# Kernel optimization log

Hardware: AMD Instinct MI355X
Metric: run time of the kernel (lower is better)

## Reference

```python
import jax, jax.numpy as jnp
import numpy as np

SIZES = [512, 2048, 4096, 8192, 16384]
BATCH = 64
MASK_DENSITY = 0.05  # GO DAG edge masks are very sparse


def setup_inputs() -> dict:
    key = jax.random.key(0)
    keys = jax.random.split(key, 1 + 3 * 4)
    inp = {"x": jax.random.normal(keys[0], (BATCH, SIZES[0]), dtype=jnp.float32)}
    for i in range(4):
        fan_in, fan_out = SIZES[i], SIZES[i + 1]
        scale = 1.0 / np.sqrt(fan_in)
        inp[f"W{i}"] = jax.random.normal(keys[1 + 3 * i], (fan_out, fan_in), dtype=jnp.float32) * scale
        inp[f"b{i}"] = jax.random.normal(keys[2 + 3 * i], (fan_out,), dtype=jnp.float32) * scale
        inp[f"mask{i}"] = jax.random.uniform(keys[3 + 3 * i], (fan_out, fan_in)) < MASK_DENSITY
    return inp


def reference(x, W0, W1, W2, W3, b0, b1, b2, b3, mask0, mask1, mask2, mask3):
    Ws = [W0, W1, W2, W3]
    bs = [b0, b1, b2, b3]
    masks = [mask0, mask1, mask2, mask3]
    n = len(Ws)
    for i in range(n):
        # SparseLinear: weight zeroed outside the GO parent-child edge mask
        Wm = Ws[i] * masks[i].astype(x.dtype)  # [out, in]
        x = x @ Wm.T + bs[i]                   # [B, out]
        if i < n - 1:
            x = jax.nn.relu(x)  # ReLU between all but the last layer
    return x
```

## Files before the change

kernel.cpp:

```cpp
#include <hip/hip_runtime.h>
#include <stdint.h>


typedef short bf16x8 __attribute__((ext_vector_type(8)));
typedef float f32x4  __attribute__((ext_vector_type(4)));

__device__ __forceinline__ unsigned short f2bf(float f) {
    unsigned int u = __float_as_uint(f);
    return (unsigned short)((u + 0x7FFFu + ((u >> 16) & 1u)) >> 16);
}

__device__ __forceinline__ unsigned int bfpair(float lo, float hi) {
    return (unsigned int)f2bf(lo) | ((unsigned int)f2bf(hi) << 16);
}

__device__ __forceinline__ bf16x8 pack8(const float4& a, const float4& b) {
    union { unsigned int u[4]; bf16x8 v; } r;
    r.u[0] = bfpair(a.x, a.y);
    r.u[1] = bfpair(a.z, a.w);
    r.u[2] = bfpair(b.x, b.y);
    r.u[3] = bfpair(b.z, b.w);
    return r.v;
}

__global__ __launch_bounds__(256) void probe_mask_kind(
    const unsigned int* __restrict__ m, int* __restrict__ flag)
{
    __shared__ int s_any;
    if (threadIdx.x == 0) s_any = 0;
    __syncthreads();
    int any = 0;
    #pragma unroll
    for (int it = 0; it < 16; ++it) {
        unsigned int v = m[it * 256 + threadIdx.x];
        if (v & 0xFFFFFF00u) any = 1;
    }
    if (__any(any) && (threadIdx.x & 63) == 0) s_any = 1;
    __syncthreads();
    if (threadIdx.x == 0) flag[0] = s_any;
}

__global__ __launch_bounds__(256) void init_bias_all(
    const float* __restrict__ b0, const float* __restrict__ b1,
    const float* __restrict__ b2, const float* __restrict__ b3,
    float* __restrict__ z0, float* __restrict__ z1,
    float* __restrict__ z2, float* __restrict__ z3)
{
    int n = blockIdx.x * 256 + threadIdx.x;
    int b = blockIdx.y;
    if (n < 2048)             z0[(size_t)b * 2048  + n]           = b0[n];
    else if (n < 6144)        z1[(size_t)b * 4096  + (n - 2048)]  = b1[n - 2048];
    else if (n < 14336)       z2[(size_t)b * 8192  + (n - 6144)]  = b2[n - 6144];
    else                      z3[(size_t)b * 16384 + (n - 14336)] = b3[n - 14336];
}

template <int MU8, int RELU>
__device__ __forceinline__ void gemm_loop(
    const float* __restrict__ X, const float* __restrict__ W,
    const unsigned char* __restrict__ Mk, const int* __restrict__ Mk32,
    int N, int K, int kbeg, int kend,
    int n0, int lr, int quad, f32x4 (&acc)[4][4])
{
    const size_t xoff = (size_t)lr * K + quad * 8;
    const size_t woff = (size_t)(n0 + lr) * K + quad * 8;

    #pragma unroll 1
    for (int k = kbeg; k < kend; k += 32) {
        bf16x8 bfr[4];
        #pragma unroll
        for (int bg = 0; bg < 4; ++bg) {
            const float* xp = X + xoff + (size_t)bg * 16 * K + k;
            float4 x0 = *(const float4*)xp;
            float4 x1 = *(const float4*)(xp + 4);
            if (RELU) {
                x0.x = fmaxf(x0.x, 0.f); x0.y = fmaxf(x0.y, 0.f);
                x0.z = fmaxf(x0.z, 0.f); x0.w = fmaxf(x0.w, 0.f);
                x1.x = fmaxf(x1.x, 0.f); x1.y = fmaxf(x1.y, 0.f);
                x1.z = fmaxf(x1.z, 0.f); x1.w = fmaxf(x1.w, 0.f);
            }
            bfr[bg] = pack8(x0, x1);
        }
        #pragma unroll
        for (int ng = 0; ng < 4; ++ng) {
            size_t e = woff + (size_t)ng * 16 * K + k;
            float4 w0 = *(const float4*)(W + e);
            float4 w1 = *(const float4*)(W + e + 4);
            if (MU8) {
                uint2 m8 = *(const uint2*)(Mk + e);
                w0.x = (m8.x & 0x000000FFu) ? w0.x : 0.f;
                w0.y = (m8.x & 0x0000FF00u) ? w0.y : 0.f;
                w0.z = (m8.x & 0x00FF0000u) ? w0.z : 0.f;
                w0.w = (m8.x & 0xFF000000u) ? w0.w : 0.f;
                w1.x = (m8.y & 0x000000FFu) ? w1.x : 0.f;
                w1.y = (m8.y & 0x0000FF00u) ? w1.y : 0.f;
                w1.z = (m8.y & 0x00FF0000u) ? w1.z : 0.f;
                w1.w = (m8.y & 0xFF000000u) ? w1.w : 0.f;
            } else {
                int4 m0 = *(const int4*)(Mk32 + e);
                int4 m1 = *(const int4*)(Mk32 + e + 4);
                w0.x = m0.x ? w0.x : 0.f;
                w0.y = m0.y ? w0.y : 0.f;
                w0.z = m0.z ? w0.z : 0.f;
                w0.w = m0.w ? w0.w : 0.f;
                w1.x = m1.x ? w1.x : 0.f;
                w1.y = m1.y ? w1.y : 0.f;
                w1.z = m1.z ? w1.z : 0.f;
                w1.w = m1.w ? w1.w : 0.f;
            }
            bf16x8 a = pack8(w0, w1);
            #pragma unroll
            for (int bg = 0; bg < 4; ++bg)
                acc[ng][bg] = __builtin_amdgcn_mfma_f32_16x16x32_bf16(
                    a, bfr[bg], acc[ng][bg], 0, 0, 0);
        }
    }
}

__global__ __launch_bounds__(64, 2) void sparse_gemm_rf(
    const float* __restrict__ X,
    const float* __restrict__ W,
    const unsigned char* __restrict__ Mk,
    const int* __restrict__ mflag,
    float* __restrict__ Z,
    int N, int K, int kper, int relu_in)
{
    const int l    = threadIdx.x;
    const int lr   = l & 15;
    const int quad = l >> 4;
    const int n0   = blockIdx.x * 64;
    const int kbeg = blockIdx.y * kper;
    const int kend = kbeg + kper;

    const int mask_u8 = *mflag;
    const int* __restrict__ Mk32 = (const int*)Mk;

    f32x4 acc[4][4];
    #pragma unroll
    for (int i = 0; i < 4; ++i)
        #pragma unroll
        for (int j = 0; j < 4; ++j) acc[i][j] = (f32x4){0.f, 0.f, 0.f, 0.f};

    if (mask_u8) {
        if (relu_in) gemm_loop<1, 1>(X, W, Mk, Mk32, N, K, kbeg, kend, n0, lr, quad, acc);
        else         gemm_loop<1, 0>(X, W, Mk, Mk32, N, K, kbeg, kend, n0, lr, quad, acc);
    } else {
        if (relu_in) gemm_loop<0, 1>(X, W, Mk, Mk32, N, K, kbeg, kend, n0, lr, quad, acc);
        else         gemm_loop<0, 0>(X, W, Mk, Mk32, N, K, kbeg, kend, n0, lr, quad, acc);
    }

    #pragma unroll
    for (int ng = 0; ng < 4; ++ng) {
        #pragma unroll
        for (int bg = 0; bg < 4; ++bg) {
            int b = bg * 16 + lr;
            float* zp = Z + (size_t)b * N + n0 + ng * 16 + quad * 4;
            #pragma unroll
            for (int r = 0; r < 4; ++r) atomicAdd(&zp[r], acc[ng][bg][r]);
        }
    }
}

extern "C" void kernel_launch(void* const* d_in, const int* in_sizes, int n_in,
                              void* d_out, int out_size, void* d_ws, size_t ws_size,
                              hipStream_t stream) {
    const float* x  = (const float*)d_in[0];
    const float* W0 = (const float*)d_in[1];
    const float* b0 = (const float*)d_in[2];
    const unsigned char* m0 = (const unsigned char*)d_in[3];
    const float* W1 = (const float*)d_in[4];
    const float* b1 = (const float*)d_in[5];
    const unsigned char* m1 = (const unsigned char*)d_in[6];
    const float* W2 = (const float*)d_in[7];
    const float* b2 = (const float*)d_in[8];
    const unsigned char* m2 = (const unsigned char*)d_in[9];
    const float* W3 = (const float*)d_in[10];
    const float* b3 = (const float*)d_in[11];
    const unsigned char* m3 = (const unsigned char*)d_in[12];

    float* z0 = (float*)d_ws;
    float* z1 = z0 + (size_t)64 * 2048;
    float* z2 = z1 + (size_t)64 * 4096;
    float* z3 = (float*)d_out;
    int* mflag = (int*)(z2 + (size_t)64 * 8192);

    probe_mask_kind<<<1, 256, 0, stream>>>((const unsigned int*)m0, mflag);
    init_bias_all<<<dim3(120, 64), 256, 0, stream>>>(b0, b1, b2, b3, z0, z1, z2, z3);

    sparse_gemm_rf<<<dim3(32, 8),  64, 0, stream>>>(x,  W0, m0, mflag, z0, 2048,  512,   64, 0);
    sparse_gemm_rf<<<dim3(64, 8),  64, 0, stream>>>(z0, W1, m1, mflag, z1, 4096,  2048, 256, 1);
    sparse_gemm_rf<<<dim3(128, 8), 64, 0, stream>>>(z1, W2, m2, mflag, z2, 8192,  4096, 512, 1);
    sparse_gemm_rf<<<dim3(256, 8), 64, 0, stream>>>(z2, W3, m3, mflag, z3, 16384, 8192, 1024, 1);
}
```

Baseline: 1.471 ms.

## Fuse all layers into one persistent cooperative kernel with grid syncs

Replaces the six separate launches (mask probe, bias init, four split-K GEMMs) with a single cooperative persistent kernel that does the probe and bias init, then loops over layers separated by grid.sync. Each wave grabs tiles in a grid-stride loop, and the split-K factor is chosen from the occupancy-derived wave count, so the K split per layer grows. This aims to remove launch gaps and to use more CUs on the large layers. The cost is grid-wide barriers and more atomic traffic from the finer K splits. The old multi-kernel path stays as a fallback if the cooperative launch fails.

Result: slower. 1.610 ms (+9.5%).

```diff
diff --git a/kernel.cpp b/kernel.cpp
--- a/kernel.cpp
+++ b/kernel.cpp
@@ -1,5 +1,8 @@
 #include <hip/hip_runtime.h>
+#include <hip/hip_cooperative_groups.h>
 #include <stdint.h>
+
+namespace cg = cooperative_groups;
 
 
 typedef short bf16x8 __attribute__((ext_vector_type(8)));
@@ -23,44 +26,13 @@
     return r.v;
 }
 
-__global__ __launch_bounds__(256) void probe_mask_kind(
-    const unsigned int* __restrict__ m, int* __restrict__ flag)
-{
-    __shared__ int s_any;
-    if (threadIdx.x == 0) s_any = 0;
-    __syncthreads();
-    int any = 0;
-    #pragma unroll
-    for (int it = 0; it < 16; ++it) {
-        unsigned int v = m[it * 256 + threadIdx.x];
-        if (v & 0xFFFFFF00u) any = 1;
-    }
-    if (__any(any) && (threadIdx.x & 63) == 0) s_any = 1;
-    __syncthreads();
-    if (threadIdx.x == 0) flag[0] = s_any;
-}
-
-__global__ __launch_bounds__(256) void init_bias_all(
-    const float* __restrict__ b0, const float* __restrict__ b1,
-    const float* __restrict__ b2, const float* __restrict__ b3,
-    float* __restrict__ z0, float* __restrict__ z1,
-    float* __restrict__ z2, float* __restrict__ z3)
-{
-    int n = blockIdx.x * 256 + threadIdx.x;
-    int b = blockIdx.y;
-    if (n < 2048)             z0[(size_t)b * 2048  + n]           = b0[n];
-    else if (n < 6144)        z1[(size_t)b * 4096  + (n - 2048)]  = b1[n - 2048];
-    else if (n < 14336)       z2[(size_t)b * 8192  + (n - 6144)]  = b2[n - 6144];
-    else                      z3[(size_t)b * 16384 + (n - 14336)] = b3[n - 14336];
-}
-
 template <int MU8, int RELU>
 __device__ __forceinline__ void gemm_loop(
     const float* __restrict__ X, const float* __restrict__ W,
-    const unsigned char* __restrict__ Mk, const int* __restrict__ Mk32,
-    int N, int K, int kbeg, int kend,
-    int n0, int lr, int quad, f32x4 (&acc)[4][4])
-{
+    const unsigned char* __restrict__ Mk,
+    int K, int kbeg, int kend, int n0, int lr, int quad, f32x4 (&acc)[4][4])
+{
+    const int* __restrict__ Mk32 = (const int*)Mk;
     const size_t xoff = (size_t)lr * K + quad * 8;
     const size_t woff = (size_t)(n0 + lr) * K + quad * 8;
 
@@ -96,16 +68,16 @@
                 w1.z = (m8.y & 0x00FF0000u) ? w1.z : 0.f;
                 w1.w = (m8.y & 0xFF000000u) ? w1.w : 0.f;
             } else {
-                int4 m0 = *(const int4*)(Mk32 + e);
-                int4 m1 = *(const int4*)(Mk32 + e + 4);
-                w0.x = m0.x ? w0.x : 0.f;
-                w0.y = m0.y ? w0.y : 0.f;
-                w0.z = m0.z ? w0.z : 0.f;
-                w0.w = m0.w ? w0.w : 0.f;
-                w1.x = m1.x ? w1.x : 0.f;
-                w1.y = m1.y ? w1.y : 0.f;
-                w1.z = m1.z ? w1.z : 0.f;
-                w1.w = m1.w ? w1.w : 0.f;
+                int4 mm0 = *(const int4*)(Mk32 + e);
+                int4 mm1 = *(const int4*)(Mk32 + e + 4);
+                w0.x = mm0.x ? w0.x : 0.f;
+                w0.y = mm0.y ? w0.y : 0.f;
+                w0.z = mm0.z ? w0.z : 0.f;
+                w0.w = mm0.w ? w0.w : 0.f;
+                w1.x = mm1.x ? w1.x : 0.f;
+                w1.y = mm1.y ? w1.y : 0.f;
+                w1.z = mm1.z ? w1.z : 0.f;
+                w1.w = mm1.w ? w1.w : 0.f;
             }
             bf16x8 a = pack8(w0, w1);
             #pragma unroll
@@ -116,37 +88,20 @@
     }
 }
 
-__global__ __launch_bounds__(64, 2) void sparse_gemm_rf(
-    const float* __restrict__ X,
-    const float* __restrict__ W,
+template <int MU8, int RELU>
+__device__ __forceinline__ void gemm_tile(
+    const float* __restrict__ X, const float* __restrict__ W,
     const unsigned char* __restrict__ Mk,
-    const int* __restrict__ mflag,
-    float* __restrict__ Z,
-    int N, int K, int kper, int relu_in)
-{
-    const int l    = threadIdx.x;
-    const int lr   = l & 15;
-    const int quad = l >> 4;
-    const int n0   = blockIdx.x * 64;
-    const int kbeg = blockIdx.y * kper;
-    const int kend = kbeg + kper;
-
-    const int mask_u8 = *mflag;
-    const int* __restrict__ Mk32 = (const int*)Mk;
-
+    float* __restrict__ Z, int N, int K,
+    int kbeg, int kend, int n0, int lr, int quad)
+{
     f32x4 acc[4][4];
     #pragma unroll
     for (int i = 0; i < 4; ++i)
         #pragma unroll
         for (int j = 0; j < 4; ++j) acc[i][j] = (f32x4){0.f, 0.f, 0.f, 0.f};
 
-    if (mask_u8) {
-        if (relu_in) gemm_loop<1, 1>(X, W, Mk, Mk32, N, K, kbeg, kend, n0, lr, quad, acc);
-        else         gemm_loop<1, 0>(X, W, Mk, Mk32, N, K, kbeg, kend, n0, lr, quad, acc);
-    } else {
-        if (relu_in) gemm_loop<0, 1>(X, W, Mk, Mk32, N, K, kbeg, kend, n0, lr, quad, acc);
-        else         gemm_loop<0, 0>(X, W, Mk, Mk32, N, K, kbeg, kend, n0, lr, quad, acc);
-    }
+    gemm_loop<MU8, RELU>(X, W, Mk, K, kbeg, kend, n0, lr, quad, acc);
 
     #pragma unroll
     for (int ng = 0; ng < 4; ++ng) {
@@ -157,6 +112,132 @@
             #pragma unroll
             for (int r = 0; r < 4; ++r) atomicAdd(&zp[r], acc[ng][bg][r]);
         }
+    }
+}
+
+template <int RELU>
+__device__ __forceinline__ void run_layer(
+    const float* __restrict__ X, const float* __restrict__ W,
+    const unsigned char* __restrict__ Mk, int mu8,
+    float* __restrict__ Z, int N, int K, int nk,
+    int wid, int nw, int lr, int quad)
+{
+    const int ntx    = N >> 6;
+    const int sh     = 31 - __clz(ntx);
+    const int kper   = K / nk;
+    const int ntiles = ntx * nk;
+    for (int t = wid; t < ntiles; t += nw) {
+        int n0   = (t & (ntx - 1)) << 6;
+        int kbeg = (t >> sh) * kper;
+        if (mu8) gemm_tile<1, RELU>(X, W, Mk, Z, N, K, kbeg, kbeg + kper, n0, lr, quad);
+        else     gemm_tile<0, RELU>(X, W, Mk, Z, N, K, kbeg, kbeg + kper, n0, lr, quad);
+    }
+}
+
+__global__ __launch_bounds__(256, 2) void fused_mlp(
+    const float* __restrict__ x,
+    const float* __restrict__ W0, const float* __restrict__ b0, const unsigned char* __restrict__ m0,
+    const float* __restrict__ W1, const float* __restrict__ b1, const unsigned char* __restrict__ m1,
+    const float* __restrict__ W2, const float* __restrict__ b2, const unsigned char* __restrict__ m2,
+    const float* __restrict__ W3, const float* __restrict__ b3, const unsigned char* __restrict__ m3,
+    float* __restrict__ z0, float* __restrict__ z1,
+    float* __restrict__ z2, float* __restrict__ z3,
+    int nk0, int nk1, int nk2, int nk3)
+{
+    cg::grid_group grid = cg::this_grid();
+
+    __shared__ int s_any;
+    if (threadIdx.x == 0) s_any = 0;
+    __syncthreads();
+    {
+        const unsigned int* mm = (const unsigned int*)m0;
+        int any = 0;
+        #pragma unroll
+        for (int it = 0; it < 16; ++it) {
+            unsigned int v = mm[it * 256 + threadIdx.x];
+            if (v & 0xFFFFFF00u) any = 1;
+        }
+        if (__any(any) && (threadIdx.x & 63) == 0) s_any = 1;
+    }
+    __syncthreads();
+    const int mu8 = s_any;
+
+    {
+        const unsigned tr = blockIdx.x * 256u + threadIdx.x;
+        const unsigned tn = gridDim.x * 256u;
+        for (unsigned i = tr; i < 64u * 2048u;  i += tn) z0[i] = b0[i & 2047u];
+        for (unsigned i = tr; i < 64u * 4096u;  i += tn) z1[i] = b1[i & 4095u];
+        for (unsigned i = tr; i < 64u * 8192u;  i += tn) z2[i] = b2[i & 8191u];
+        for (unsigned i = tr; i < 64u * 16384u; i += tn) z3[i] = b3[i & 16383u];
+    }
+
+    grid.sync();
+
+    const int wid  = (blockIdx.x << 2) | (threadIdx.x >> 6);
+    const int nw   = gridDim.x << 2;
+    const int l    = threadIdx.x & 63;
+    const int lr   = l & 15;
+    const int quad = l >> 4;
+
+    run_layer<0>(x,  W0, m0, mu8, z0, 2048,  512,  nk0, wid, nw, lr, quad);
+    grid.sync();
+    run_layer<1>(z0, W1, m1, mu8, z1, 4096,  2048, nk1, wid, nw, lr, quad);
+    grid.sync();
+    run_layer<1>(z1, W2, m2, mu8, z2, 8192,  4096, nk2, wid, nw, lr, quad);
+    grid.sync();
+    run_layer<1>(z2, W3, m3, mu8, z3, 16384, 8192, nk3, wid, nw, lr, quad);
+}
+
+
+__global__ __launch_bounds__(256) void probe_mask_kind(
+    const unsigned int* __restrict__ m, int* __restrict__ flag)
+{
+    __shared__ int s_any;
+    if (threadIdx.x == 0) s_any = 0;
+    __syncthreads();
+    int any = 0;
+    #pragma unroll
+    for (int it = 0; it < 16; ++it) {
+        unsigned int v = m[it * 256 + threadIdx.x];
+        if (v & 0xFFFFFF00u) any = 1;
+    }
+    if (__any(any) && (threadIdx.x & 63) == 0) s_any = 1;
+    __syncthreads();
+    if (threadIdx.x == 0) flag[0] = s_any;
+}
+
+__global__ __launch_bounds__(256) void init_bias_all(
+    const float* __restrict__ b0, const float* __restrict__ b1,
+    const float* __restrict__ b2, const float* __restrict__ b3,
+    float* __restrict__ z0, float* __restrict__ z1,
+    float* __restrict__ z2, float* __restrict__ z3)
+{
+    int n = blockIdx.x * 256 + threadIdx.x;
+    int b = blockIdx.y;
+    if (n < 2048)             z0[(size_t)b * 2048  + n]           = b0[n];
+    else if (n < 6144)        z1[(size_t)b * 4096  + (n - 2048)]  = b1[n - 2048];
+    else if (n < 14336)       z2[(size_t)b * 8192  + (n - 6144)]  = b2[n - 6144];
+    else                      z3[(size_t)b * 16384 + (n - 14336)] = b3[n - 14336];
+}
+
+__global__ __launch_bounds__(64, 2) void sparse_gemm_rf(
+    const float* __restrict__ X, const float* __restrict__ W,
+    const unsigned char* __restrict__ Mk, const int* __restrict__ mflag,
+    float* __restrict__ Z, int N, int K, int kper, int relu_in)
+{
+    const int l    = threadIdx.x;
+    const int lr   = l & 15;
+    const int quad = l >> 4;
+    const int n0   = blockIdx.x * 64;
+    const int kbeg = blockIdx.y * kper;
+    const int mu8  = *mflag;
+
+    if (mu8) {
+        if (relu_in) gemm_tile<1, 1>(X, W, Mk, Z, N, K, kbeg, kbeg + kper, n0, lr, quad);
+        else         gemm_tile<1, 0>(X, W, Mk, Z, N, K, kbeg, kbeg + kper, n0, lr, quad);
+    } else {
+        if (relu_in) gemm_tile<0, 1>(X, W, Mk, Z, N, K, kbeg, kbeg + kper, n0, lr, quad);
+        else         gemm_tile<0, 0>(X, W, Mk, Z, N, K, kbeg, kbeg + kper, n0, lr, quad);
     }
 }
 
@@ -181,13 +262,48 @@
     float* z1 = z0 + (size_t)64 * 2048;
     float* z2 = z1 + (size_t)64 * 4096;
     float* z3 = (float*)d_out;
-    int* mflag = (int*)(z2 + (size_t)64 * 8192);
-
-    probe_mask_kind<<<1, 256, 0, stream>>>((const unsigned int*)m0, mflag);
-    init_bias_all<<<dim3(120, 64), 256, 0, stream>>>(b0, b1, b2, b3, z0, z1, z2, z3);
-
-    sparse_gemm_rf<<<dim3(32, 8),  64, 0, stream>>>(x,  W0, m0, mflag, z0, 2048,  512,   64, 0);
-    sparse_gemm_rf<<<dim3(64, 8),  64, 0, stream>>>(z0, W1, m1, mflag, z1, 4096,  2048, 256, 1);
-    sparse_gemm_rf<<<dim3(128, 8), 64, 0, stream>>>(z1, W2, m2, mflag, z2, 8192,  4096, 512, 1);
-    sparse_gemm_rf<<<dim3(256, 8), 64, 0, stream>>>(z2, W3, m3, mflag, z3, 16384, 8192, 1024, 1);
-}
+
+    static int blocksPerCU = -1;
+    if (blocksPerCU < 0) {
+        hipError_t e = hipOccupancyMaxActiveBlocksPerMultiprocessor(
+            &blocksPerCU, reinterpret_cast<const void*>(&fused_mlp), 256, 0);
+        if (e != hipSuccess || blocksPerCU <= 0) blocksPerCU = 2;
+        if (blocksPerCU > 8) blocksPerCU = 8;
+    }
+    int G = blocksPerCU * 256;
+    if (G > 2048) G = 2048;
+    const int WV = G * 4;
+
+    auto pick_nk = [&](int ntx, int K) {
+        int nk = 1;
+        while (ntx * nk < WV && (K / (nk * 2)) >= 64) nk <<= 1;
+        return nk;
+    };
+    int nk0 = pick_nk(32,  512);
+    int nk1 = pick_nk(64,  2048);
+    int nk2 = pick_nk(128, 4096);
+    int nk3 = pick_nk(256, 8192);
+
+    void* args[] = {
+        (void*)&x,
+        (void*)&W0, (void*)&b0, (void*)&m0,
+        (void*)&W1, (void*)&b1, (void*)&m1,
+        (void*)&W2, (void*)&b2, (void*)&m2,
+        (void*)&W3, (void*)&b3, (void*)&m3,
+        (void*)&z0, (void*)&z1, (void*)&z2, (void*)&z3,
+        (void*)&nk0, (void*)&nk1, (void*)&nk2, (void*)&nk3
+    };
+    hipError_t le = hipLaunchCooperativeKernel(
+        reinterpret_cast<const void*>(&fused_mlp),
+        dim3(G), dim3(256), args, 0, stream);
+
+    if (le != hipSuccess) {
+        int* mflag = (int*)(z2 + (size_t)64 * 8192);
+        probe_mask_kind<<<1, 256, 0, stream>>>((const unsigned int*)m0, mflag);
+        init_bias_all<<<dim3(120, 64), 256, 0, stream>>>(b0, b1, b2, b3, z0, z1, z2, z3);
+        sparse_gemm_rf<<<dim3(32, 8),  64, 0, stream>>>(x,  W0, m0, mflag, z0, 2048,  512,   64, 0);
+        sparse_gemm_rf<<<dim3(64, 8),  64, 0, stream>>>(z0, W1, m1, mflag, z1, 4096,  2048, 256, 1);
+        sparse_gemm_rf<<<dim3(128, 8), 64, 0, stream>>>(z1, W2, m2, mflag, z2, 8192,  4096, 512, 1);
+        sparse_gemm_rf<<<dim3(256, 8), 64, 0, stream>>>(z2, W3, m3, mflag, z3, 16384, 8192, 1024, 1);
+    }
+}
```
